# Kernel optimization log

Hardware: AMD Instinct MI355X
Metric: run time of the kernel (lower is better)

The kernel has to match this reference:

```python
import jax, jax.numpy as jnp
import numpy as np

SIZE = 7
SIGMA = 1.5
K1 = 0.01
K2 = 0.03
DATA_RANGE = 2.0
NP_ = SIZE * SIZE
COV_NORM = NP_ / (NP_ - 1)
PAD = SIZE // 2


def _gaussian_window(size=SIZE, sigma=SIGMA, channels=1):
    x = np.arange(size) - size // 2
    g = np.exp(-x**2 / (2.0 * sigma**2))[None, :]
    g = (g.T @ g)
    g = g / g.sum()
    w = np.tile(g[None, None], (channels, 1, 1, 1))  # [C,1,size,size]
    return jnp.asarray(w, dtype=jnp.float32)


def _dwconv(x, w):
    # depthwise conv2d, zero padding PAD, stride 1; x: [N,C,H,W], w: [C,1,k,k]
    c = x.shape[1]
    return jax.lax.conv_general_dilated(
        x, w, window_strides=(1, 1), padding=[(PAD, PAD), (PAD, PAD)],
        dimension_numbers=('NCHW', 'OIHW', 'NCHW'), feature_group_count=c)


def setup_inputs() -> dict:
    key = jax.random.key(0)
    k1, k2 = jax.random.split(key)
    X = jax.random.uniform(k1, (64, 1, 320, 320), dtype=jnp.float32)
    Y = jax.random.uniform(k2, (64, 1, 320, 320), dtype=jnp.float32)
    window = _gaussian_window()
    return {"X": X, "Y": Y, "window": window}


def reference(X, Y, window):
    C1 = (K1 * DATA_RANGE) ** 2
    C2 = (K2 * DATA_RANGE) ** 2
    mux = _dwconv(X, window)
    muy = _dwconv(Y, window)
    mux_sq = mux * mux
    muy_sq = muy * muy
    muxy = mux * muy
    sigmax_sq = (_dwconv(X * X, window) - mux_sq) * COV_NORM
    sigmay_sq = (_dwconv(Y * Y, window) - muy_sq) * COV_NORM
    sigmaxy = (_dwconv(X * Y, window) - muxy) * COV_NORM
    ssim_map = ((2 * muxy + C1) * (2 * sigmaxy + C2)) / \
               ((mux_sq + muy_sq + C1) * (sigmax_sq + sigmay_sq + C2))
    return 1.0 - ssim_map.mean()
```

## Files before the change

kernel.cpp:

```cpp
#include <hip/hip_runtime.h>
#include <math.h>


#define WI 320
#define HI 320
#define NI 64
#define TWO 58
#define GXD 6
#define SROWS 32
#define ITERS 4
#define WPB 2
#define RPB (WPB * SROWS)
#define GYD (HI / RPB)
#define NBLK (GXD * GYD * NI)
#define NPART (NBLK * WPB)
#define NPIX ((double)NI * WI * HI)

#define MU_OFF 0
#define SQ_OFF 1088
#define XY_OFF 2176
#define WAVE_LDS 2752

typedef float v2 __attribute__((ext_vector_type(2)));
typedef float v4 __attribute__((ext_vector_type(4)));

struct W7 { float w[7]; };

__device__ __forceinline__ v2 pget(const v4* t, int p) {
    v4 q = t[p >> 1];
    return (p & 1) ? (v2){q.z, q.w} : (v2){q.x, q.y};
}
__device__ __forceinline__ float sget(const v4* t, int p) {
    v4 q = t[p >> 2];
    switch (p & 3) { case 0: return q.x; case 1: return q.y; case 2: return q.z; default: return q.w; }
}

__global__ __launch_bounds__(WPB * 64) void ssim_kernel(
    const float* __restrict__ X, const float* __restrict__ Y,
    W7 wv, float* __restrict__ partial)
{
    __shared__ __align__(16) float lds_all[WPB * WAVE_LDS + 16];

    const int tid  = threadIdx.x;
    const int lane = tid & 63;
    const int wid  = tid >> 6;
    float* lds = lds_all + wid * WAVE_LDS;

    const int x0 = blockIdx.x * TWO;
    const int y0 = blockIdx.y * RPB + wid * SROWS;
    const float* __restrict__ Xn = X + (size_t)blockIdx.z * (WI * HI);
    const float* __restrict__ Yn = Y + (size_t)blockIdx.z * (WI * HI);

    const int  gx   = x0 + lane - 3;
    const bool xok  = (unsigned)gx < (unsigned)WI;
    const int  gxc  = min(max(gx, 0), WI - 1);
    const int  maxc = min(TWO, WI - x0);

    v2 win[14];
#pragma unroll
    for (int k = 0; k < 6; ++k) {
        const int gy  = y0 - 3 + k;
        const bool ok = xok && ((unsigned)gy < (unsigned)HI);
        const int gyc = min(max(gy, 0), HI - 1);
        const size_t idx = (size_t)gyc * WI + gxc;
        v2 t; t.x = Xn[idx]; t.y = Yn[idx];
        win[k] = ok ? t : (v2){0.f, 0.f};
    }

    const float C1 = 0.0004f, C2 = 0.0036f, COVN = 49.f / 48.f;
    const int row = lane >> 3;
    const int g   = lane & 7;

    float lsum = 0.f;
#pragma unroll 1
    for (int it = 0; it < ITERS; ++it) {
        const int base_row = y0 + it * 8;

#pragma unroll
        for (int k = 0; k < 8; ++k) {
            const int gy  = base_row + 3 + k;
            const bool ok = xok && ((unsigned)gy < (unsigned)HI);
            const int gyc = min(max(gy, 0), HI - 1);
            const size_t idx = (size_t)gyc * WI + gxc;
            v2 t; t.x = Xn[idx]; t.y = Yn[idx];
            win[6 + k] = ok ? t : (v2){0.f, 0.f};
        }

        v2 amu[8], asq[8]; float axy[8];
#pragma unroll
        for (int r = 0; r < 8; ++r) { amu[r] = (v2){0.f,0.f}; asq[r] = (v2){0.f,0.f}; axy[r] = 0.f; }
#pragma unroll
        for (int k = 0; k < 14; ++k) {
            const v2 v   = win[k];
            const v2 sq  = v * v;
            const float pxy = v.x * v.y;
#pragma unroll
            for (int r = 0; r < 8; ++r) {
                const int d = k - r;
                if (d >= 0 && d < 7) {
                    const float w = wv.w[d];
                    amu[r] += w * v;
                    asq[r] += w * sq;
                    axy[r] += w * pxy;
                }
            }
        }

#pragma unroll
        for (int r = 0; r < 8; ++r) {
            *(v2*)&lds[MU_OFF + r * 136 + 2 * lane] = amu[r];
            *(v2*)&lds[SQ_OFF + r * 136 + 2 * lane] = asq[r];
            lds[XY_OFF + r * 68 + lane] = axy[r];
        }
        __builtin_amdgcn_wave_barrier();

        v2 mmu[8], msq[8]; float mxy[8];
#pragma unroll
        for (int j = 0; j < 8; ++j) { mmu[j] = (v2){0.f,0.f}; msq[j] = (v2){0.f,0.f}; mxy[j] = 0.f; }
        {
            v4 t[8];
#pragma unroll
            for (int q = 0; q < 8; ++q)
                t[q] = *(const v4*)&lds[MU_OFF + row * 136 + 16 * g + 4 * q];
#pragma unroll
            for (int j = 0; j < 8; ++j)
#pragma unroll
                for (int d = 0; d < 7; ++d)
                    mmu[j] += wv.w[d] * pget(t, j + d);
        }
        {
            v4 t[8];
#pragma unroll
            for (int q = 0; q < 8; ++q)
                t[q] = *(const v4*)&lds[SQ_OFF + row * 136 + 16 * g + 4 * q];
#pragma unroll
            for (int j = 0; j < 8; ++j)
#pragma unroll
                for (int d = 0; d < 7; ++d)
                    msq[j] += wv.w[d] * pget(t, j + d);
        }
        {
            v4 t[4];
#pragma unroll
            for (int q = 0; q < 4; ++q)
                t[q] = *(const v4*)&lds[XY_OFF + row * 68 + 8 * g + 4 * q];
#pragma unroll
            for (int j = 0; j < 8; ++j)
#pragma unroll
                for (int d = 0; d < 7; ++d)
                    mxy[j] += wv.w[d] * sget(t, j + d);
        }

#pragma unroll
        for (int j = 0; j < 8; ++j) {
            const v2 mu    = mmu[j];
            const v2 musq  = mu * mu;
            const float pm = mu.x * mu.y;
            const v2 sig   = (msq[j] - musq) * COVN;
            const float vxy = (mxy[j] - pm) * COVN;
            const float num = (2.f * pm + C1) * (2.f * vxy + C2);
            const float den = (musq.x + musq.y + C1) * (sig.x + sig.y + C2);
            lsum += (8 * g + j < maxc) ? num * __builtin_amdgcn_rcpf(den) : 0.f;
        }

#pragma unroll
        for (int k = 0; k < 6; ++k) win[k] = win[k + 8];
    }

#pragma unroll
    for (int off = 32; off > 0; off >>= 1)
        lsum += __shfl_down(lsum, off, 64);
    if (lane == 0) {
        const int bid = ((blockIdx.z * GYD + blockIdx.y) * GXD + blockIdx.x) * WPB + wid;
        partial[bid] = lsum;
    }
}

__global__ __launch_bounds__(256) void ssim_finalize(
    const float* __restrict__ partial, float* __restrict__ out)
{
    __shared__ double ws[4];
    const int tid = threadIdx.x;
    double s = 0.0;
    for (int i = tid; i < NPART; i += 256) s += (double)partial[i];
#pragma unroll
    for (int off = 32; off > 0; off >>= 1)
        s += __shfl_down(s, off, 64);
    if ((tid & 63) == 0) ws[tid >> 6] = s;
    __syncthreads();
    if (tid == 0)
        out[0] = (float)(1.0 - ((ws[0] + ws[1]) + (ws[2] + ws[3])) / NPIX);
}

extern "C" void kernel_launch(void* const* d_in, const int* in_sizes, int n_in,
                              void* d_out, int out_size, void* d_ws, size_t ws_size,
                              hipStream_t stream) {
    const float* X = (const float*)d_in[0];
    const float* Y = (const float*)d_in[1];
    W7 wv;
    {
        double gk[7], s = 0.0;
        for (int i = 0; i < 7; ++i) {
            double x = (double)(i - 3);
            gk[i] = exp(-(x * x) / (2.0 * 1.5 * 1.5));
            s += gk[i];
        }
        for (int i = 0; i < 7; ++i) wv.w[i] = (float)(gk[i] / s);
    }

    float* partial = (float*)d_ws;

    dim3 grid(GXD, GYD, NI);
    ssim_kernel<<<grid, WPB * 64, 0, stream>>>(X, Y, wv, partial);
    ssim_finalize<<<1, 256, 0, stream>>>(partial, (float*)d_out);
}
```

Before: 110.8 us.

## Process four rows per iteration with 60-lane horizontal pass

Each wave now computes 4 output rows per iteration instead of 8, halving the strip height to 16 rows so the grid has twice as many blocks. The horizontal pass maps 60 lanes to (row, 4-column) tiles instead of 64 lanes to 8-column tiles, and per-wave LDS shrinks accordingly. The aim is more parallelism, higher occupancy and lower register pressure, at the cost of more redundant vertical halo loads (10 rows loaded per 4 outputs instead of 14 per 8) and 4 idle lanes during the horizontal pass.

```diff
diff --git a/kernel.cpp b/kernel.cpp
--- a/kernel.cpp
+++ b/kernel.cpp
@@ -7,7 +7,7 @@
 #define NI 64
 #define TWO 58
 #define GXD 6
-#define SROWS 32
+#define SROWS 16
 #define ITERS 4
 #define WPB 2
 #define RPB (WPB * SROWS)
@@ -17,20 +17,20 @@
 #define NPIX ((double)NI * WI * HI)
 
 #define MU_OFF 0
-#define SQ_OFF 1088
-#define XY_OFF 2176
-#define WAVE_LDS 2752
+#define SQ_OFF 544
+#define XY_OFF 1088
+#define WAVE_LDS 1368
 
 typedef float v2 __attribute__((ext_vector_type(2)));
 typedef float v4 __attribute__((ext_vector_type(4)));
 
 struct W7 { float w[7]; };
 
-__device__ __forceinline__ v2 pget(const v4* t, int p) {
+__device__ __forceinline__ v2 pget5(const v4* t, int p) {
     v4 q = t[p >> 1];
     return (p & 1) ? (v2){q.z, q.w} : (v2){q.x, q.y};
 }
-__device__ __forceinline__ float sget(const v4* t, int p) {
+__device__ __forceinline__ float sget3(const v4* t, int p) {
     v4 q = t[p >> 2];
     switch (p & 3) { case 0: return q.x; case 1: return q.y; case 2: return q.z; default: return q.w; }
 }
@@ -39,7 +39,7 @@
     const float* __restrict__ X, const float* __restrict__ Y,
     W7 wv, float* __restrict__ partial)
 {
-    __shared__ __align__(16) float lds_all[WPB * WAVE_LDS + 16];
+    __shared__ __align__(16) float lds_all[WPB * WAVE_LDS];
 
     const int tid  = threadIdx.x;
     const int lane = tid & 63;
@@ -56,7 +56,13 @@
     const int  gxc  = min(max(gx, 0), WI - 1);
     const int  maxc = min(TWO, WI - x0);
 
-    v2 win[14];
+    const bool act  = lane < 60;
+    const int  hrow = lane / 15;
+    const int  c0   = (lane % 15) * 4;
+
+    const float C1 = 0.0004f, C2 = 0.0036f, COVN = 49.f / 48.f;
+
+    v2 win[10];
 #pragma unroll
     for (int k = 0; k < 6; ++k) {
         const int gy  = y0 - 3 + k;
@@ -67,18 +73,14 @@
         win[k] = ok ? t : (v2){0.f, 0.f};
     }
 
-    const float C1 = 0.0004f, C2 = 0.0036f, COVN = 49.f / 48.f;
-    const int row = lane >> 3;
-    const int g   = lane & 7;
-
     float lsum = 0.f;
 #pragma unroll 1
     for (int it = 0; it < ITERS; ++it) {
-        const int base_row = y0 + it * 8;
-
-#pragma unroll
-        for (int k = 0; k < 8; ++k) {
-            const int gy  = base_row + 3 + k;
+        const int base = y0 + 4 * it;
+
+#pragma unroll
+        for (int k = 0; k < 4; ++k) {
+            const int gy  = base + 3 + k;
             const bool ok = xok && ((unsigned)gy < (unsigned)HI);
             const int gyc = min(max(gy, 0), HI - 1);
             const size_t idx = (size_t)gyc * WI + gxc;
@@ -86,16 +88,16 @@
             win[6 + k] = ok ? t : (v2){0.f, 0.f};
         }
 
-        v2 amu[8], asq[8]; float axy[8];
-#pragma unroll
-        for (int r = 0; r < 8; ++r) { amu[r] = (v2){0.f,0.f}; asq[r] = (v2){0.f,0.f}; axy[r] = 0.f; }
-#pragma unroll
-        for (int k = 0; k < 14; ++k) {
-            const v2 v   = win[k];
-            const v2 sq  = v * v;
+        v2 amu[4], asq[4]; float axy[4];
+#pragma unroll
+        for (int r = 0; r < 4; ++r) { amu[r] = (v2){0.f,0.f}; asq[r] = (v2){0.f,0.f}; axy[r] = 0.f; }
+#pragma unroll
+        for (int k = 0; k < 10; ++k) {
+            const v2 v = win[k];
+            const v2 sq = v * v;
             const float pxy = v.x * v.y;
 #pragma unroll
-            for (int r = 0; r < 8; ++r) {
+            for (int r = 0; r < 4; ++r) {
                 const int d = k - r;
                 if (d >= 0 && d < 7) {
                     const float w = wv.w[d];
@@ -107,64 +109,65 @@
         }
 
 #pragma unroll
-        for (int r = 0; r < 8; ++r) {
+        for (int r = 0; r < 4; ++r) {
             *(v2*)&lds[MU_OFF + r * 136 + 2 * lane] = amu[r];
             *(v2*)&lds[SQ_OFF + r * 136 + 2 * lane] = asq[r];
             lds[XY_OFF + r * 68 + lane] = axy[r];
         }
         __builtin_amdgcn_wave_barrier();
 
-        v2 mmu[8], msq[8]; float mxy[8];
-#pragma unroll
-        for (int j = 0; j < 8; ++j) { mmu[j] = (v2){0.f,0.f}; msq[j] = (v2){0.f,0.f}; mxy[j] = 0.f; }
-        {
-            v4 t[8];
-#pragma unroll
-            for (int q = 0; q < 8; ++q)
-                t[q] = *(const v4*)&lds[MU_OFF + row * 136 + 16 * g + 4 * q];
-#pragma unroll
-            for (int j = 0; j < 8; ++j)
-#pragma unroll
-                for (int d = 0; d < 7; ++d)
-                    mmu[j] += wv.w[d] * pget(t, j + d);
-        }
-        {
-            v4 t[8];
-#pragma unroll
-            for (int q = 0; q < 8; ++q)
-                t[q] = *(const v4*)&lds[SQ_OFF + row * 136 + 16 * g + 4 * q];
-#pragma unroll
-            for (int j = 0; j < 8; ++j)
-#pragma unroll
-                for (int d = 0; d < 7; ++d)
-                    msq[j] += wv.w[d] * pget(t, j + d);
-        }
-        {
-            v4 t[4];
-#pragma unroll
-            for (int q = 0; q < 4; ++q)
-                t[q] = *(const v4*)&lds[XY_OFF + row * 68 + 8 * g + 4 * q];
-#pragma unroll
-            for (int j = 0; j < 8; ++j)
-#pragma unroll
-                for (int d = 0; d < 7; ++d)
-                    mxy[j] += wv.w[d] * sget(t, j + d);
-        }
-
-#pragma unroll
-        for (int j = 0; j < 8; ++j) {
-            const v2 mu    = mmu[j];
-            const v2 musq  = mu * mu;
-            const float pm = mu.x * mu.y;
-            const v2 sig   = (msq[j] - musq) * COVN;
-            const float vxy = (mxy[j] - pm) * COVN;
-            const float num = (2.f * pm + C1) * (2.f * vxy + C2);
-            const float den = (musq.x + musq.y + C1) * (sig.x + sig.y + C2);
-            lsum += (8 * g + j < maxc) ? num * __builtin_amdgcn_rcpf(den) : 0.f;
-        }
-
-#pragma unroll
-        for (int k = 0; k < 6; ++k) win[k] = win[k + 8];
+        if (act) {
+            v2 mmu[4], msq[4]; float mxy[4];
+#pragma unroll
+            for (int j = 0; j < 4; ++j) { mmu[j] = (v2){0.f,0.f}; msq[j] = (v2){0.f,0.f}; mxy[j] = 0.f; }
+            {
+                v4 t[5];
+#pragma unroll
+                for (int q = 0; q < 5; ++q)
+                    t[q] = *(const v4*)&lds[MU_OFF + hrow * 136 + 2 * c0 + 4 * q];
+#pragma unroll
+                for (int j = 0; j < 4; ++j)
+#pragma unroll
+                    for (int d = 0; d < 7; ++d)
+                        mmu[j] += wv.w[d] * pget5(t, j + d);
+            }
+            {
+                v4 t[5];
+#pragma unroll
+                for (int q = 0; q < 5; ++q)
+                    t[q] = *(const v4*)&lds[SQ_OFF + hrow * 136 + 2 * c0 + 4 * q];
+#pragma unroll
+                for (int j = 0; j < 4; ++j)
+#pragma unroll
+                    for (int d = 0; d < 7; ++d)
+                        msq[j] += wv.w[d] * pget5(t, j + d);
+            }
+            {
+                v4 u[3];
+#pragma unroll
+                for (int q = 0; q < 3; ++q)
+                    u[q] = *(const v4*)&lds[XY_OFF + hrow * 68 + c0 + 4 * q];
+#pragma unroll
+                for (int j = 0; j < 4; ++j)
+#pragma unroll
+                    for (int d = 0; d < 7; ++d)
+                        mxy[j] += wv.w[d] * sget3(u, j + d);
+            }
+#pragma unroll
+            for (int j = 0; j < 4; ++j) {
+                const v2 mu   = mmu[j];
+                const v2 musq = mu * mu;
+                const float pm  = mu.x * mu.y;
+                const v2 sig  = (msq[j] - musq) * COVN;
+                const float vxy = (mxy[j] - pm) * COVN;
+                const float num = (2.f * pm + C1) * (2.f * vxy + C2);
+                const float den = (musq.x + musq.y + C1) * (sig.x + sig.y + C2);
+                lsum += (c0 + j < maxc) ? num * __builtin_amdgcn_rcpf(den) : 0.f;
+            }
+        }
+
+#pragma unroll
+        for (int k = 0; k < 6; ++k) win[k] = win[k + 4];
     }
 
 #pragma unroll
```

New measurement: 111.3 us. No clear change (+0.4%).
